# Kernel optimization log

Measured on AMD Instinct MI355X. Metric: run time of the kernel, lower is better.

## Reference

```python
import math
import jax, jax.numpy as jnp
import numpy as np

BSZ, SEQ, DIM = 2, 2048, 4096
N_HEADS, N_KV = 32, 8
HEAD_DIM = DIM // N_HEADS  # 128
N_REP = N_HEADS // N_KV    # 4
EPS = 1e-5
ROPE_THETA = 500000.0


def setup_inputs() -> dict:
    key = jax.random.key(0)
    ks = jax.random.split(key, 6)
    scale = 0.02
    x = jax.random.normal(ks[0], (BSZ, SEQ, DIM), dtype=jnp.float32)
    wq = jax.random.normal(ks[1], (N_HEADS * HEAD_DIM, DIM), dtype=jnp.float32) * scale
    wk = jax.random.normal(ks[2], (N_KV * HEAD_DIM, DIM), dtype=jnp.float32) * scale
    wv = jax.random.normal(ks[3], (N_KV * HEAD_DIM, DIM), dtype=jnp.float32) * scale
    wo = jax.random.normal(ks[4], (N_HEADS * HEAD_DIM, DIM), dtype=jnp.float32).T * scale  # [DIM, n_heads*hd] -> stored as [out,in]
    wo = jax.random.normal(ks[4], (DIM, N_HEADS * HEAD_DIM), dtype=jnp.float32) * scale
    # RoPE tables (real/imag parts of freqs_cis)
    inv_freq = 1.0 / (ROPE_THETA ** (jnp.arange(0, HEAD_DIM, 2, dtype=jnp.float32) / HEAD_DIM))
    angles = jnp.arange(SEQ, dtype=jnp.float32)[:, None] * inv_freq[None, :]  # [SEQ, HEAD_DIM//2]
    cos, sin = jnp.cos(angles), jnp.sin(angles)
    # causal additive mask
    neg_inf = jnp.finfo(jnp.float32).min
    mask = jnp.where(jnp.tril(jnp.ones((SEQ, SEQ), dtype=bool)), 0.0, neg_inf).astype(jnp.float32)
    return {"x": x, "wq": wq, "wk": wk, "wv": wv, "wo": wo,
            "cos": cos, "sin": sin, "mask": mask, "start_pos": 0}


def _apply_rope(t, cos, sin):
    # t: [b, s, h, hd]; pairs (even, odd) as in view_as_complex
    tf = t.astype(jnp.float32).reshape(*t.shape[:-1], HEAD_DIM // 2, 2)
    e, o = tf[..., 0], tf[..., 1]
    c = cos[None, :, None, :]
    s = sin[None, :, None, :]
    out = jnp.stack([e * c - o * s, e * s + o * c], axis=-1)
    return out.reshape(t.shape).astype(t.dtype)


def _rmsnorm(t):
    tf = t.astype(jnp.float32)
    return (tf * jax.lax.rsqrt(jnp.mean(tf * tf, axis=-1, keepdims=True) + EPS)).astype(t.dtype)


def reference(x, wq, wk, wv, wo, cos, sin, mask, start_pos):
    b, s, _ = x.shape
    xq = (x @ wq.T).reshape(b, s, N_HEADS, HEAD_DIM)
    xk = (x @ wk.T).reshape(b, s, N_KV, HEAD_DIM)
    xv = (x @ wv.T).reshape(b, s, N_KV, HEAD_DIM)
    xq = _apply_rope(xq, cos, sin)
    xk = _apply_rope(xk, cos, sin)
    xq = _rmsnorm(xq)
    xk = _rmsnorm(xk)
    # KV cache write/read with start_pos=0 over seqlen tokens is identity here.
    # GQA without repeat_interleave: q head h attends kv head h // N_REP
    q = xq.transpose(0, 2, 1, 3).reshape(b, N_KV, N_REP, s, HEAD_DIM)
    k = xk.transpose(0, 2, 1, 3)  # [b, n_kv, s, hd]
    v = xv.transpose(0, 2, 1, 3)
    scale = 1.0 / math.sqrt(HEAD_DIM)
    scores = jnp.einsum('bgrqd,bgkd->bgrqk', q, k) * scale + mask[None, None, None]
    probs = jax.nn.softmax(scores, axis=-1)
    out = jnp.einsum('bgrqk,bgkd->bgrqd', probs, v)
    out = out.reshape(b, N_HEADS, s, HEAD_DIM).transpose(0, 2, 1, 3).reshape(b, s, N_HEADS * HEAD_DIM)
    return out @ wo.T
```

## Files before the change

### kernel.cpp

```cpp
#include <hip/hip_runtime.h>
#include <hip/hip_bf16.h>
#include <stdint.h>

#define SEQ 2048
#define DIMSZ 4096
#define QKVN 6144

typedef __attribute__((ext_vector_type(8))) __bf16 bf16x8;
typedef __attribute__((ext_vector_type(4))) float f32x4;

static __device__ __forceinline__ void gld_lds16(const void* g, void* l) {
  __builtin_amdgcn_global_load_lds(
      (__attribute__((address_space(1))) void*)(g),
      (__attribute__((address_space(3))) void*)(l), 16, 0, 0);
}

static __device__ __forceinline__ void blockbar() {
  asm volatile("" ::: "memory");
  __builtin_amdgcn_s_barrier();
  asm volatile("" ::: "memory");
}

__global__ __launch_bounds__(256) void k_cvt(const float* __restrict__ in,
                                             __bf16* __restrict__ out, long n) {
  long i = (long)blockIdx.x * 256 + threadIdx.x;
  long stride = (long)gridDim.x * 256;
  for (long e = i * 8; e < n; e += stride * 8) {
    float4 v0 = *(const float4*)(in + e);
    float4 v1 = *(const float4*)(in + e + 4);
    bf16x8 o;
    o[0] = (__bf16)v0.x; o[1] = (__bf16)v0.y; o[2] = (__bf16)v0.z; o[3] = (__bf16)v0.w;
    o[4] = (__bf16)v1.x; o[5] = (__bf16)v1.y; o[6] = (__bf16)v1.z; o[7] = (__bf16)v1.w;
    *(bf16x8*)(out + e) = o;
  }
}

template <typename OutT>
__global__ __launch_bounds__(512) void k_gemm256(const __bf16* __restrict__ A,
                                                 const __bf16* __restrict__ B,
                                                 OutT* __restrict__ C,
                                                 int M, int N, int K) {
  __shared__ __align__(16) __bf16 As[2][2][128 * 64];
  __shared__ __align__(16) __bf16 Bs[2][2][128 * 64];
  const int t = threadIdx.x;
  const int l = t & 63;
  const int w = t >> 6;
  const int wm = w >> 2;
  const int wn = w & 3;
  const int lr = l & 15, lg = l >> 4;
  const int sw = lr & 7;
  const int bm = blockIdx.y, bn = blockIdx.x;

  const int srow = t >> 3;
  const int scol = ((t & 7) ^ (srow & 7)) << 3;
  const __bf16* pa0 = A + (size_t)(bm * 256 +   0 + srow) * K + scol;
  const __bf16* pa1 = A + (size_t)(bm * 256 +  64 + srow) * K + scol;
  const __bf16* pa2 = A + (size_t)(bm * 256 + 128 + srow) * K + scol;
  const __bf16* pa3 = A + (size_t)(bm * 256 + 192 + srow) * K + scol;
  const __bf16* pb0 = B + (size_t)(bn * 256 +   0 + srow) * K + scol;
  const __bf16* pb1 = B + (size_t)(bn * 256 +  64 + srow) * K + scol;
  const __bf16* pb2 = B + (size_t)(bn * 256 + 128 + srow) * K + scol;
  const __bf16* pb3 = B + (size_t)(bn * 256 + 192 + srow) * K + scol;
  const int ldst = t * 8;

#define STAGE_A(buf, kc)                              \
  do {                                                \
    gld_lds16(pa0 + (kc), &As[buf][0][ldst]);         \
    gld_lds16(pa1 + (kc), &As[buf][0][4096 + ldst]);  \
    gld_lds16(pa2 + (kc), &As[buf][1][ldst]);         \
    gld_lds16(pa3 + (kc), &As[buf][1][4096 + ldst]);  \
  } while (0)
#define STAGE_B0(buf, kc)                             \
  do {                                                \
    gld_lds16(pb0 + (kc), &Bs[buf][0][ldst]);         \
    gld_lds16(pb1 + (kc), &Bs[buf][0][4096 + ldst]);  \
  } while (0)
#define STAGE_B1(buf, kc)                             \
  do {                                                \
    gld_lds16(pb2 + (kc), &Bs[buf][1][ldst]);         \
    gld_lds16(pb3 + (kc), &Bs[buf][1][4096 + ldst]);  \
  } while (0)

  const int c0 = ((lg ^ sw) * 8);
  const int c1 = (((lg ^ sw) ^ 4) * 8);
  const int aRow = lr;
  const int bRow = (wn & 1) * 64 + lr;

  f32x4 acc[8][4] = {};
  const int nt = K >> 6;

  STAGE_A(0, 0);
  STAGE_B0(0, 0);
  STAGE_B1(0, 0);
  STAGE_A(1, (nt > 1 ? 64 : 0));
  asm volatile("s_waitcnt vmcnt(4)" ::: "memory");
  blockbar();

  for (int T = 0; T < nt; ++T) {
    const int cur = T & 1;
    const int kB = (T + 1 < nt ? T + 1 : nt - 1) << 6;
    const int kA = (T + 2 < nt ? T + 2 : nt - 1) << 6;
    bf16x8 a[4][2], b0[2][2], b1[2][2];

#pragma unroll
    for (int mi = 0; mi < 4; ++mi) {
      a[mi][0] = *(const bf16x8*)&As[cur][wm][(mi * 16 + aRow) * 64 + c0];
      a[mi][1] = *(const bf16x8*)&As[cur][wm][(mi * 16 + aRow) * 64 + c1];
    }
#pragma unroll
    for (int ni = 0; ni < 2; ++ni) {
      b0[ni][0] = *(const bf16x8*)&Bs[cur][wn >> 1][(ni * 16 + bRow) * 64 + c0];
      b0[ni][1] = *(const bf16x8*)&Bs[cur][wn >> 1][(ni * 16 + bRow) * 64 + c1];
    }
    STAGE_B0((T + 1) & 1, kB);
    blockbar();
    __builtin_amdgcn_s_setprio(1);
#pragma unroll
    for (int mi = 0; mi < 4; ++mi)
#pragma unroll
      for (int ni = 0; ni < 2; ++ni)
#pragma unroll
        for (int kk = 0; kk < 2; ++kk)
          acc[mi][ni] = __builtin_amdgcn_mfma_f32_16x16x32_bf16(a[mi][kk], b0[ni][kk], acc[mi][ni], 0, 0, 0);
    __builtin_amdgcn_s_setprio(0);
    blockbar();

#pragma unroll
    for (int ni = 0; ni < 2; ++ni) {
      b1[ni][0] = *(const bf16x8*)&Bs[cur][wn >> 1][((ni + 2) * 16 + bRow) * 64 + c0];
      b1[ni][1] = *(const bf16x8*)&Bs[cur][wn >> 1][((ni + 2) * 16 + bRow) * 64 + c1];
    }
    STAGE_B1((T + 1) & 1, kB);
    blockbar();
    __builtin_amdgcn_s_setprio(1);
#pragma unroll
    for (int mi = 0; mi < 4; ++mi)
#pragma unroll
      for (int ni = 0; ni < 2; ++ni)
#pragma unroll
        for (int kk = 0; kk < 2; ++kk)
          acc[mi][ni + 2] = __builtin_amdgcn_mfma_f32_16x16x32_bf16(a[mi][kk], b1[ni][kk], acc[mi][ni + 2], 0, 0, 0);
    __builtin_amdgcn_s_setprio(0);
    blockbar();

#pragma unroll
    for (int mi = 0; mi < 4; ++mi) {
      a[mi][0] = *(const bf16x8*)&As[cur][wm][((mi + 4) * 16 + aRow) * 64 + c0];
      a[mi][1] = *(const bf16x8*)&As[cur][wm][((mi + 4) * 16 + aRow) * 64 + c1];
    }
    blockbar();
    __builtin_amdgcn_s_setprio(1);
#pragma unroll
    for (int mi = 0; mi < 4; ++mi)
#pragma unroll
      for (int ni = 0; ni < 2; ++ni)
#pragma unroll
        for (int kk = 0; kk < 2; ++kk)
          acc[mi + 4][ni + 2] = __builtin_amdgcn_mfma_f32_16x16x32_bf16(a[mi][kk], b1[ni][kk], acc[mi + 4][ni + 2], 0, 0, 0);
    __builtin_amdgcn_s_setprio(0);
    blockbar();

    STAGE_A(cur, kA);
    blockbar();
    __builtin_amdgcn_s_setprio(1);
#pragma unroll
    for (int mi = 0; mi < 4; ++mi)
#pragma unroll
      for (int ni = 0; ni < 2; ++ni)
#pragma unroll
        for (int kk = 0; kk < 2; ++kk)
          acc[mi + 4][ni] = __builtin_amdgcn_mfma_f32_16x16x32_bf16(a[mi][kk], b0[ni][kk], acc[mi + 4][ni], 0, 0, 0);
    __builtin_amdgcn_s_setprio(0);
    asm volatile("s_waitcnt vmcnt(4)" ::: "memory");
    blockbar();
  }
#undef STAGE_A
#undef STAGE_B0
#undef STAGE_B1

  const int row0 = bm * 256 + wm * 128;
  const int col0 = bn * 256 + wn * 64;
#pragma unroll
  for (int mi = 0; mi < 8; ++mi)
#pragma unroll
    for (int ni = 0; ni < 4; ++ni)
#pragma unroll
      for (int r = 0; r < 4; ++r)
        C[(size_t)(row0 + mi * 16 + lg * 4 + r) * N + (col0 + ni * 16 + lr)] =
            (OutT)acc[mi][ni][r];
}

__global__ __launch_bounds__(256) void k_rope_norm(__bf16* __restrict__ qkv,
                                                   const float* __restrict__ cosT,
                                                   const float* __restrict__ sinT) {
  const int task = blockIdx.x * 4 + (threadIdx.x >> 6);
  const int l = threadIdx.x & 63;
  const int m = task / 40;
  const int h = task - m * 40;
  const int s = m & (SEQ - 1);
  const bool isQ = h < 32;
  const int col = isQ ? h * 128 : 4096 + (h - 32) * 128;
  __bf16* p = qkv + (size_t)m * QKVN + col + l * 2;
  float e = (float)p[0], o = (float)p[1];
  float c = cosT[s * 64 + l], sn = sinT[s * 64 + l];
  float e2 = e * c - o * sn;
  float o2 = e * sn + o * c;
  float ss = e2 * e2 + o2 * o2;
#pragma unroll
  for (int off = 32; off > 0; off >>= 1) ss += __shfl_xor(ss, off);
  float r = rsqrtf(ss * (1.0f / 128.0f) + 1e-5f);
  if (isQ) r *= 0.08838834764831845f;
  p[0] = (__bf16)(e2 * r);
  p[1] = (__bf16)(o2 * r);
}

__global__ __launch_bounds__(256) void k_transpose_v(const __bf16* __restrict__ qkv,
                                                     __bf16* __restrict__ vt) {
  __shared__ __bf16 tile[64][136];
  const int t = threadIdx.x;
  const int st = blockIdx.x, bg = blockIdx.y;
  const int b = bg >> 3, g = bg & 7;
  const int s0 = st * 64;
#pragma unroll
  for (int p = 0; p < 4; ++p) {
    int row = p * 16 + (t >> 4);
    int co = (t & 15) * 8;
    *(bf16x8*)&tile[row][co] =
        *(const bf16x8*)&qkv[(size_t)(b * SEQ + s0 + row) * QKVN + 5120 + g * 128 + co];
  }
  __syncthreads();
#pragma unroll
  for (int p = 0; p < 4; ++p) {
    int d = p * 32 + (t >> 3);
    int so = (t & 7) * 8;
    bf16x8 v;
#pragma unroll
    for (int j = 0; j < 8; ++j) v[j] = tile[so + j][d];
    *(bf16x8*)&vt[((size_t)bg * 128 + d) * SEQ + s0 + so] = v;
  }
}

__global__ __launch_bounds__(256) void k_flash(const __bf16* __restrict__ qkv,
                                               const __bf16* __restrict__ vt,
                                               __bf16* __restrict__ attno) {
  __shared__ __bf16 Ks[64 * 128];
  __shared__ __bf16 Vs[128 * 64];
  __shared__ __bf16 Ps[4][16 * 64];
  const int t = threadIdx.x, w = t >> 6, l = t & 63;
  const int lr = l & 15, lg = l >> 4;
  const int bh = blockIdx.y;
  const int b = bh >> 5, h = bh & 31, g = h >> 2;
  const int qt0 = blockIdx.x, qt1 = 31 - (int)blockIdx.x;

  const __bf16* Kb = qkv + 4096 + (size_t)(b * SEQ) * QKVN + g * 128;
  const __bf16* Vtb = vt + ((size_t)(b * 8 + g)) * 128 * SEQ;
  const int wbase = (t & ~63) * 8;
  const int sw = lr & 7;

  for (int pass = 0; pass < 2; ++pass) {
    const int qt = (pass == 0) ? qt0 : qt1;

    const __bf16* Qb = qkv + (size_t)(b * SEQ + qt * 64 + w * 16 + lr) * QKVN + h * 128;
    bf16x8 qf[4];
#pragma unroll
    for (int kk = 0; kk < 4; ++kk) qf[kk] = *(const bf16x8*)&Qb[kk * 32 + lg * 8];

    f32x4 oacc[8] = {};
    float mrow[4], lsum[4];
#pragma unroll
    for (int r = 0; r < 4; ++r) { mrow[r] = -1e30f; lsum[r] = 0.f; }

    for (int kt = 0; kt <= qt; ++kt) {
      const int kv0 = kt * 64;
#pragma unroll
      for (int i = 0; i < 4; ++i) {
        int e = i * 256 + t;
        gld_lds16(Kb + (size_t)(kv0 + (e >> 4)) * QKVN + ((e & 15) ^ ((e >> 4) & 7)) * 8,
                  &Ks[i * 2048 + wbase]);
      }
#pragma unroll
      for (int i = 0; i < 4; ++i) {
        int e = i * 256 + t;
        gld_lds16(Vtb + (size_t)(e >> 3) * SEQ + kv0 + (((e & 7) ^ ((e >> 3) & 7))) * 8,
                  &Vs[i * 2048 + wbase]);
      }
      __syncthreads();

      f32x4 sc[4] = {};
#pragma unroll
      for (int kk = 0; kk < 4; ++kk)
#pragma unroll
        for (int n = 0; n < 4; ++n) {
          bf16x8 kf = *(const bf16x8*)&Ks[(n * 16 + lr) * 128 + ((kk * 4 + lg) ^ sw) * 8];
          sc[n] = __builtin_amdgcn_mfma_f32_16x16x32_bf16(qf[kk], kf, sc[n], 0, 0, 0);
        }

      if (kt == qt) {
#pragma unroll
        for (int n = 0; n < 4; ++n)
#pragma unroll
          for (int r = 0; r < 4; ++r)
            if (n * 16 + lr > w * 16 + lg * 4 + r) sc[n][r] = -1e30f;
      }

#pragma unroll
      for (int r = 0; r < 4; ++r) {
        float pm = fmaxf(fmaxf(sc[0][r], sc[1][r]), fmaxf(sc[2][r], sc[3][r]));
#pragma unroll
        for (int off = 8; off > 0; off >>= 1) pm = fmaxf(pm, __shfl_xor(pm, off));
        float mn = fmaxf(mrow[r], pm);
        float corr = __expf(mrow[r] - mn);
        mrow[r] = mn;
        float ps = 0.f;
#pragma unroll
        for (int n = 0; n < 4; ++n) { sc[n][r] = __expf(sc[n][r] - mn); ps += sc[n][r]; }
#pragma unroll
        for (int off = 8; off > 0; off >>= 1) ps += __shfl_xor(ps, off);
        lsum[r] = lsum[r] * corr + ps;
#pragma unroll
        for (int dn = 0; dn < 8; ++dn) oacc[dn][r] *= corr;
      }

#pragma unroll
      for (int n = 0; n < 4; ++n)
#pragma unroll
        for (int r = 0; r < 4; ++r) {
          int row = lg * 4 + r;
          Ps[w][row * 64 + (((n * 2 + (lr >> 3)) ^ (row & 7)) * 8) + (lr & 7)] = (__bf16)sc[n][r];
        }

#pragma unroll
      for (int ks = 0; ks < 2; ++ks) {
        bf16x8 pf = *(const bf16x8*)&Ps[w][lr * 64 + ((ks * 4 + lg) ^ sw) * 8];
#pragma unroll
        for (int dn = 0; dn < 8; ++dn) {
          bf16x8 vf = *(const bf16x8*)&Vs[(dn * 16 + lr) * 64 + ((ks * 4 + lg) ^ sw) * 8];
          oacc[dn] = __builtin_amdgcn_mfma_f32_16x16x32_bf16(pf, vf, oacc[dn], 0, 0, 0);
        }
      }
      __syncthreads();
    }

    __bf16* Ob = attno + (size_t)(b * SEQ + qt * 64 + w * 16) * DIMSZ + h * 128;
#pragma unroll
    for (int dn = 0; dn < 8; ++dn)
#pragma unroll
      for (int r = 0; r < 4; ++r)
        Ob[(size_t)(lg * 4 + r) * DIMSZ + dn * 16 + lr] = (__bf16)(oacc[dn][r] / lsum[r]);
  }
}

extern "C" void kernel_launch(void* const* d_in, const int* in_sizes, int n_in,
                              void* d_out, int out_size, void* d_ws, size_t ws_size,
                              hipStream_t stream) {
  const float* x    = (const float*)d_in[0];
  const float* wq   = (const float*)d_in[1];
  const float* wk   = (const float*)d_in[2];
  const float* wv   = (const float*)d_in[3];
  const float* wo   = (const float*)d_in[4];
  const float* cosT = (const float*)d_in[5];
  const float* sinT = (const float*)d_in[6];

  char* ws = (char*)d_ws;
  __bf16* xb    = (__bf16*)(ws);
  __bf16* wqkvb = (__bf16*)(ws + 33554432);
  __bf16* qkvb  = (__bf16*)(ws + 83886080);
  __bf16* wob   = (__bf16*)(ws + 134217728);
  __bf16* vt    = (__bf16*)(ws + 167772160);
  __bf16* attno = (__bf16*)(ws + 176160768);
  float* out = (float*)d_out;

  k_cvt<<<8192, 256, 0, stream>>>(x, xb, 16777216L);
  k_cvt<<<8192, 256, 0, stream>>>(wq, wqkvb, 16777216L);
  k_cvt<<<2048, 256, 0, stream>>>(wk, wqkvb + 16777216, 4194304L);
  k_cvt<<<2048, 256, 0, stream>>>(wv, wqkvb + 20971520, 4194304L);
  k_cvt<<<8192, 256, 0, stream>>>(wo, wob, 16777216L);

  k_gemm256<__bf16><<<dim3(24, 16), 512, 0, stream>>>(xb, wqkvb, qkvb, 4096, QKVN, 4096);
  k_rope_norm<<<40960, 256, 0, stream>>>(qkvb, cosT, sinT);
  k_transpose_v<<<dim3(32, 16), 256, 0, stream>>>(qkvb, vt);
  k_flash<<<dim3(16, 64), 256, 0, stream>>>(qkvb, vt, attno);
  k_gemm256<float><<<dim3(16, 16), 512, 0, stream>>>(attno, wob, out, 4096, DIMSZ, 4096);
}
```

Baseline: 631.0 us.

## Add lazy softmax rescaling, hoist load addressing, set MFMA priority in flash kernel

```diff
diff --git a/kernel.cpp b/kernel.cpp
--- a/kernel.cpp
+++ b/kernel.cpp
@@ -252,8 +252,10 @@
   const int b = bh >> 5, h = bh & 31, g = h >> 2;
   const int qt0 = blockIdx.x, qt1 = 31 - (int)blockIdx.x;
 
-  const __bf16* Kb = qkv + 4096 + (size_t)(b * SEQ) * QKVN + g * 128;
-  const __bf16* Vtb = vt + ((size_t)(b * 8 + g)) * 128 * SEQ;
+  const __bf16* kp = qkv + 4096 + (size_t)(b * SEQ + (t >> 4)) * QKVN + g * 128 +
+                     (((t & 15) ^ ((t >> 4) & 7)) * 8);
+  const __bf16* vp = vt + (size_t)(b * 8 + g) * 128 * SEQ + (size_t)(t >> 3) * SEQ +
+                     (((t & 7) ^ ((t >> 3) & 7)) * 8);
   const int wbase = (t & ~63) * 8;
   const int sw = lr & 7;
 
@@ -271,22 +273,17 @@
     for (int r = 0; r < 4; ++r) { mrow[r] = -1e30f; lsum[r] = 0.f; }
 
     for (int kt = 0; kt <= qt; ++kt) {
-      const int kv0 = kt * 64;
-#pragma unroll
-      for (int i = 0; i < 4; ++i) {
-        int e = i * 256 + t;
-        gld_lds16(Kb + (size_t)(kv0 + (e >> 4)) * QKVN + ((e & 15) ^ ((e >> 4) & 7)) * 8,
-                  &Ks[i * 2048 + wbase]);
-      }
-#pragma unroll
-      for (int i = 0; i < 4; ++i) {
-        int e = i * 256 + t;
-        gld_lds16(Vtb + (size_t)(e >> 3) * SEQ + kv0 + (((e & 7) ^ ((e >> 3) & 7))) * 8,
-                  &Vs[i * 2048 + wbase]);
-      }
+      const size_t kv0 = (size_t)kt * 64;
+#pragma unroll
+      for (int i = 0; i < 4; ++i)
+        gld_lds16(kp + (kv0 + i * 16) * QKVN, &Ks[i * 2048 + wbase]);
+#pragma unroll
+      for (int i = 0; i < 4; ++i)
+        gld_lds16(vp + (size_t)i * 32 * SEQ + kv0, &Vs[i * 2048 + wbase]);
       __syncthreads();
 
       f32x4 sc[4] = {};
+      __builtin_amdgcn_s_setprio(1);
 #pragma unroll
       for (int kk = 0; kk < 4; ++kk)
 #pragma unroll
@@ -294,6 +291,7 @@
           bf16x8 kf = *(const bf16x8*)&Ks[(n * 16 + lr) * 128 + ((kk * 4 + lg) ^ sw) * 8];
           sc[n] = __builtin_amdgcn_mfma_f32_16x16x32_bf16(qf[kk], kf, sc[n], 0, 0, 0);
         }
+      __builtin_amdgcn_s_setprio(0);
 
       if (kt == qt) {
 #pragma unroll
@@ -303,22 +301,41 @@
             if (n * 16 + lr > w * 16 + lg * 4 + r) sc[n][r] = -1e30f;
       }
 
+      float pml[4];
+      float need = -1e30f;
 #pragma unroll
       for (int r = 0; r < 4; ++r) {
-        float pm = fmaxf(fmaxf(sc[0][r], sc[1][r]), fmaxf(sc[2][r], sc[3][r]));
-#pragma unroll
-        for (int off = 8; off > 0; off >>= 1) pm = fmaxf(pm, __shfl_xor(pm, off));
-        float mn = fmaxf(mrow[r], pm);
-        float corr = __expf(mrow[r] - mn);
-        mrow[r] = mn;
-        float ps = 0.f;
-#pragma unroll
-        for (int n = 0; n < 4; ++n) { sc[n][r] = __expf(sc[n][r] - mn); ps += sc[n][r]; }
-#pragma unroll
-        for (int off = 8; off > 0; off >>= 1) ps += __shfl_xor(ps, off);
-        lsum[r] = lsum[r] * corr + ps;
-#pragma unroll
-        for (int dn = 0; dn < 8; ++dn) oacc[dn][r] *= corr;
+        pml[r] = fmaxf(fmaxf(sc[0][r], sc[1][r]), fmaxf(sc[2][r], sc[3][r]));
+        need = fmaxf(need, pml[r] - mrow[r]);
+      }
+      if (__all(need <= 8.0f)) {
+#pragma unroll
+        for (int r = 0; r < 4; ++r) {
+          float ps = 0.f;
+#pragma unroll
+          for (int n = 0; n < 4; ++n) { sc[n][r] = __expf(sc[n][r] - mrow[r]); ps += sc[n][r]; }
+#pragma unroll
+          for (int off = 8; off > 0; off >>= 1) ps += __shfl_xor(ps, off);
+          lsum[r] += ps;
+        }
+      } else {
+#pragma unroll
+        for (int r = 0; r < 4; ++r) {
+          float pm = pml[r];
+#pragma unroll
+          for (int off = 8; off > 0; off >>= 1) pm = fmaxf(pm, __shfl_xor(pm, off));
+          float mn = fmaxf(mrow[r], pm);
+          float corr = __expf(mrow[r] - mn);
+          mrow[r] = mn;
+          float ps = 0.f;
+#pragma unroll
+          for (int n = 0; n < 4; ++n) { sc[n][r] = __expf(sc[n][r] - mn); ps += sc[n][r]; }
+#pragma unroll
+          for (int off = 8; off > 0; off >>= 1) ps += __shfl_xor(ps, off);
+          lsum[r] = lsum[r] * corr + ps;
+#pragma unroll
+          for (int dn = 0; dn < 8; ++dn) oacc[dn][r] *= corr;
+        }
       }
 
 #pragma unroll
@@ -329,6 +346,7 @@
           Ps[w][row * 64 + (((n * 2 + (lr >> 3)) ^ (row & 7)) * 8) + (lr & 7)] = (__bf16)sc[n][r];
         }
 
+      __builtin_amdgcn_s_setprio(1);
 #pragma unroll
       for (int ks = 0; ks < 2; ++ks) {
         bf16x8 pf = *(const bf16x8*)&Ps[w][lr * 64 + ((ks * 4 + lg) ^ sw) * 8];
@@ -338,15 +356,19 @@
           oacc[dn] = __builtin_amdgcn_mfma_f32_16x16x32_bf16(pf, vf, oacc[dn], 0, 0, 0);
         }
       }
+      __builtin_amdgcn_s_setprio(0);
       __syncthreads();
     }
 
+    float inv[4];
+#pragma unroll
+    for (int r = 0; r < 4; ++r) inv[r] = __builtin_amdgcn_rcpf(lsum[r]);
     __bf16* Ob = attno + (size_t)(b * SEQ + qt * 64 + w * 16) * DIMSZ + h * 128;
 #pragma unroll
     for (int dn = 0; dn < 8; ++dn)
 #pragma unroll
       for (int r = 0; r < 4; ++r)
-        Ob[(size_t)(lg * 4 + r) * DIMSZ + dn * 16 + lr] = (__bf16)(oacc[dn][r] / lsum[r]);
+        Ob[(size_t)(lg * 4 + r) * DIMSZ + dn * 16 + lr] = (__bf16)(oacc[dn][r] * inv[r]);
   }
 }
 
```

New measurement: 613.7 us. -2.7%, faster.
